# Kernel optimization log

Hardware: AMD Instinct MI355X
Metric: run time of the kernel (lower is better)

## Reference

```python
import jax, jax.numpy as jnp
import numpy as np

D_MODEL = 512
N_HEADS = 8
D_HEAD = D_MODEL // N_HEADS
B, S = 4, 2048
NEG_INF = -1e9


def rel_shift(x):
    # x: [B,H,Q,K] -> Transformer-XL relative shift
    b, h, q, k = x.shape
    x = jnp.pad(x, ((0, 0), (0, 0), (0, 0), (1, 0)))  # [B,H,Q,K+1]
    x = x.reshape(b, h, k + 1, q)[:, :, 1:, :]          # drop first row
    return x.reshape(b, h, q, k)


def setup_inputs() -> dict:
    key = jax.random.key(0)
    ks = jax.random.split(key, 9)
    sc = 1.0 / np.sqrt(D_MODEL)
    return {
        "x": jax.random.normal(ks[0], (B, S, D_MODEL), jnp.float32),
        "pos_emb": jax.random.normal(ks[1], (S, D_MODEL), jnp.float32),
        "Wq": jax.random.normal(ks[2], (D_MODEL, D_MODEL), jnp.float32) * sc,
        "Wk": jax.random.normal(ks[3], (D_MODEL, D_MODEL), jnp.float32) * sc,
        "Wv": jax.random.normal(ks[4], (D_MODEL, D_MODEL), jnp.float32) * sc,
        "Wr": jax.random.normal(ks[5], (D_MODEL, D_MODEL), jnp.float32) * sc,
        "Wo": jax.random.normal(ks[6], (D_MODEL, D_MODEL), jnp.float32) * sc,
        "u_bias": jax.random.normal(ks[7], (N_HEADS, D_HEAD), jnp.float32) * 0.02,
        "v_bias": jax.random.normal(ks[8], (N_HEADS, D_HEAD), jnp.float32) * 0.02,
    }


def reference(x, pos_emb, Wq, Wk, Wv, Wr, Wo, u_bias, v_bias):
    b, s, _ = x.shape
    # projections -> [B,S,H,Dh]; relative pos -> [S,H,Dh]
    q = (x @ Wq).reshape(b, s, N_HEADS, D_HEAD)
    k = (x @ Wk).reshape(b, s, N_HEADS, D_HEAD)
    v = (x @ Wv).reshape(b, s, N_HEADS, D_HEAD)
    r = (pos_emb @ Wr).reshape(s, N_HEADS, D_HEAD)

    # content term (AC) and position term (BD, with rel shift)
    ac = jnp.einsum("bihd,bjhd->bhij", q + u_bias, k)
    bd = rel_shift(jnp.einsum("bihd,jhd->bhij", q + v_bias, r))

    scores = (ac + bd) / np.sqrt(D_HEAD)
    causal = jnp.tril(jnp.ones((s, s), bool))
    scores = jnp.where(causal, scores, NEG_INF)
    attn = jax.nn.softmax(scores, axis=-1)  # [B,H,S,S]

    out = jnp.einsum("bhij,bjhd->bihd", attn, v).reshape(b, s, D_MODEL)
    return out @ Wo
```

## Files before the change

kernel.cpp:

```cpp
#include <hip/hip_runtime.h>
#include <math.h>

#define SS 2048
#define BB 4
#define NHD 8
#define BH (BB * NHD)

typedef float f32x4 __attribute__((ext_vector_type(4)));
typedef __bf16 bf16x8 __attribute__((ext_vector_type(8)));

__device__ __forceinline__ short f2bf(float x) {
  unsigned u = __float_as_uint(x);
  unsigned r = (u + 0x7fffu + ((u >> 16) & 1u)) >> 16;
  return (short)r;
}

__device__ __forceinline__ void gld16(const void* g, void* l) {
  __builtin_amdgcn_global_load_lds(
      (const __attribute__((address_space(1))) unsigned int*)g,
      (__attribute__((address_space(3))) unsigned int*)l, 16, 0, 0);
}

__global__ void cast_bf16(const float* __restrict__ in, short* __restrict__ out) {
  int i = blockIdx.x * blockDim.x + threadIdx.x;
  float4 v = ((const float4*)in)[i];
  ((short4*)out)[i] = make_short4(f2bf(v.x), f2bf(v.y), f2bf(v.z), f2bf(v.w));
}

__global__ __launch_bounds__(256) void castT_w(
    const float* __restrict__ W0, const float* __restrict__ W1,
    const float* __restrict__ W2, const float* __restrict__ W3,
    const float* __restrict__ W4, short* __restrict__ T0, short* __restrict__ T1,
    short* __restrict__ T2, short* __restrict__ T3, short* __restrict__ T4) {
  __shared__ float t[64][65];
  const float* W;
  short* T;
  switch (blockIdx.z) {
    case 0: W = W0; T = T0; break;
    case 1: W = W1; T = T1; break;
    case 2: W = W2; T = T2; break;
    case 3: W = W3; T = T3; break;
    default: W = W4; T = T4; break;
  }
  const int k0 = blockIdx.x * 64, n0 = blockIdx.y * 64;
  const int tid = threadIdx.x;
#pragma unroll
  for (int rep = 0; rep < 4; rep++) {
    int idx = rep * 256 + tid;
    int r = idx >> 4, c4 = (idx & 15) << 2;
    float4 v = *(const float4*)&W[(size_t)(k0 + r) * 512 + n0 + c4];
    t[r][c4] = v.x; t[r][c4 + 1] = v.y; t[r][c4 + 2] = v.z; t[r][c4 + 3] = v.w;
  }
  __syncthreads();
#pragma unroll
  for (int rep = 0; rep < 4; rep++) {
    int idx = rep * 256 + tid;
    int n = idx >> 4, k4 = (idx & 15) << 2;
    short4 s = make_short4(f2bf(t[k4][n]), f2bf(t[k4 + 1][n]),
                           f2bf(t[k4 + 2][n]), f2bf(t[k4 + 3][n]));
    *(short4*)&T[(size_t)(n0 + n) * 512 + k0 + k4] = s;
  }
}

__global__ __launch_bounds__(256) void conv_vt(const short* __restrict__ Vh,
                                               short* __restrict__ Vt) {
  __shared__ short t[64][72];
  const int s0 = blockIdx.x * 64, bh = blockIdx.y, tid = threadIdx.x;
#pragma unroll
  for (int rep = 0; rep < 4; rep++) {
    int idx = rep * 256 + tid;
    int r = idx >> 4, c4 = (idx & 15) << 2;
    *(short4*)&t[r][c4] = *(const short4*)&Vh[((size_t)bh * SS + s0 + r) * 64 + c4];
  }
  __syncthreads();
#pragma unroll
  for (int rep = 0; rep < 4; rep++) {
    int idx = rep * 256 + tid;
    int d = idx >> 4, s4 = (idx & 15) << 2;
    short4 o = make_short4(t[s4][d], t[s4 + 1][d], t[s4 + 2][d], t[s4 + 3][d]);
    *(short4*)&Vt[((size_t)bh * 64 + d) * SS + s0 + s4] = o;
  }
}

template <int EPI>
__global__ __launch_bounds__(512) void mfma_gemm(
    const short* __restrict__ A, const short* __restrict__ Bt, int M,
    short* __restrict__ o0, short* __restrict__ o1,
    const float* __restrict__ bias0, const float* __restrict__ bias1,
    float* __restrict__ of) {
  __shared__ short lds[2][2][128 * 64];
  const int m0 = blockIdx.x * 128;
  const int n0 = blockIdx.y * 128;
  const int tid = threadIdx.x;
  const int lane = tid & 63;
  const int w = tid >> 6;
  const int wr = w >> 2, wc = w & 3;
  const int g = lane >> 4, li = lane & 15;

  f32x4 acc[4][2] = {};

  auto stage = [&](int buf, int k0) {
#pragma unroll
    for (int i = 0; i < 2; i++) {
      int p = (i * 512 + tid) * 16;
      int q = p ^ ((p >> 3) & 0x70);
      int row = q >> 7, col = (q & 127) >> 1;
      gld16(A + (size_t)(m0 + row) * 512 + k0 + col, (char*)&lds[buf][0][0] + p);
      gld16(Bt + (size_t)(n0 + row) * 512 + k0 + col, (char*)&lds[buf][1][0] + p);
    }
  };

  stage(0, 0);
  __syncthreads();
  int buf = 0;
  for (int t = 0; t < 8; t++) {
    if (t < 7) stage(buf ^ 1, (t + 1) * 64);
    const char* As = (const char*)&lds[buf][0][0];
    const char* Bs = (const char*)&lds[buf][1][0];
    bf16x8 af[4][2], bfr[2][2];
#pragma unroll
    for (int ks = 0; ks < 2; ks++) {
      const int cb = g * 16 + ks * 64;
#pragma unroll
      for (int mi = 0; mi < 4; mi++) {
        int row = wr * 64 + mi * 16 + li;
        af[mi][ks] = *(const bf16x8*)(As + row * 128 + (cb ^ ((row & 7) << 4)));
      }
#pragma unroll
      for (int ni = 0; ni < 2; ni++) {
        int row = wc * 32 + ni * 16 + li;
        bfr[ni][ks] = *(const bf16x8*)(Bs + row * 128 + (cb ^ ((row & 7) << 4)));
      }
    }
#pragma unroll
    for (int ks = 0; ks < 2; ks++)
#pragma unroll
      for (int mi = 0; mi < 4; mi++)
#pragma unroll
        for (int ni = 0; ni < 2; ni++)
          acc[mi][ni] = __builtin_amdgcn_mfma_f32_16x16x32_bf16(
              af[mi][ks], bfr[ni][ks], acc[mi][ni], 0, 0, 0);
    __syncthreads();
    buf ^= 1;
  }

#pragma unroll
  for (int mi = 0; mi < 4; mi++) {
#pragma unroll
    for (int ni = 0; ni < 2; ni++) {
      const int n_g = n0 + wc * 32 + ni * 16 + li;
      const int m_b = m0 + wr * 64 + mi * 16 + g * 4;
      if (EPI == 0) {
#pragma unroll
        for (int r = 0; r < 4; r++)
          of[(size_t)(m_b + r) * 512 + n_g] = acc[mi][ni][r];
      } else if (EPI == 1) {
        const float b0 = bias0[n_g], b1 = bias1[n_g];
        const int h = n_g >> 6, d = n_g & 63;
#pragma unroll
        for (int r = 0; r < 4; r++) {
          int m_g = m_b + r;
          size_t ad = ((size_t)((m_g >> 11) * NHD + h) * SS + (m_g & 2047)) * 64 + d;
          o0[ad] = f2bf(acc[mi][ni][r] + b0);
          o1[ad] = f2bf(acc[mi][ni][r] + b1);
        }
      } else {
        const int h = n_g >> 6, d = n_g & 63;
#pragma unroll
        for (int r = 0; r < 4; r++) {
          int m_g = m_b + r;
          size_t ad = ((size_t)((m_g >> 11) * NHD + h) * SS + (m_g & 2047)) * 64 + d;
          o0[ad] = f2bf(acc[mi][ni][r]);
        }
      }
    }
  }
}

__global__ __launch_bounds__(512, 4) void flash_mfma_kernel(
    const short* __restrict__ Qu_, const short* __restrict__ Qv_,
    const short* __restrict__ Kb_, const short* __restrict__ Vt_,
    const short* __restrict__ Rb_, short* __restrict__ AOb) {
  __shared__ __align__(16) float QRl[8][80 * 18];
  __shared__ __align__(16) short Pl[8][16 * 72];

  const int bx = blockIdx.x;
  const int bh = blockIdx.y;
  const int h = bh & 7;
  const int tid = threadIdx.x;
  const int w = tid >> 6;
  const int wq = w & 3;
  const int qi = (w < 4) ? (31 - bx) : bx;
  const int i0 = qi * 64;
  const int lane = tid & 63;
  const int q = lane & 15;
  const int g = lane >> 4;
  const int dsl = g * 8;

  float* qrw = QRl[w];
  short* pw = Pl[w];

  const size_t qoff = ((size_t)bh * SS + (i0 + wq * 16 + q)) * 64;
  bf16x8 quF[2], qvF[2];
  quF[0] = *(const bf16x8*)(Qu_ + qoff + dsl);
  quF[1] = *(const bf16x8*)(Qu_ + qoff + dsl + 32);
  qvF[0] = *(const bf16x8*)(Qv_ + qoff + dsl);
  qvF[1] = *(const bf16x8*)(Qv_ + qoff + dsl + 32);

  const int i_my = i0 + wq * 16 + q;

  float m = -1e30f, l = 0.f;
  f32x4 o[4] = {};

  for (int j0 = 0; j0 <= i0; j0 += 64) {
    bf16x8 vf[4][2];
    const size_t vtb = ((size_t)bh * 64) * SS + j0;
#pragma unroll
    for (int ds = 0; ds < 4; ds++)
#pragma unroll
      for (int c = 0; c < 2; c++)
        vf[ds][c] = *(const bf16x8*)(Vt_ + vtb + (size_t)(ds * 16 + q) * SS + dsl + 32 * c);

    f32x4 accS[4] = {};
    f32x4 accR[5] = {};
    const size_t kbase = ((size_t)bh * SS + j0) * 64;
    const int rb0 = SS - 16 + j0 - i0 - 16 * wq;
    const size_t rbase = (size_t)h * SS * 64;
#pragma unroll
    for (int c = 0; c < 2; c++) {
      const int dof = dsl + 32 * c;
#pragma unroll
      for (int ks = 0; ks < 4; ks++) {
        bf16x8 kf = *(const bf16x8*)(Kb_ + kbase + (size_t)(ks * 16 + q) * 64 + dof);
        accS[ks] = __builtin_amdgcn_mfma_f32_16x16x32_bf16(kf, quF[c], accS[ks], 0, 0, 0);
      }
#pragma unroll
      for (int st = 0; st < 5; st++) {
        int rrow = rb0 + st * 16 + q;
        rrow = rrow < SS ? rrow : SS - 1;
        bf16x8 rf = *(const bf16x8*)(Rb_ + rbase + (size_t)rrow * 64 + dof);
        accR[st] = __builtin_amdgcn_mfma_f32_16x16x32_bf16(rf, qvF[c], accR[st], 0, 0, 0);
      }
    }

#pragma unroll
    for (int st = 0; st < 5; st++)
#pragma unroll
      for (int r = 0; r < 4; r++)
        qrw[(st * 16 + g * 4 + r) * 18 + q] = accR[st][r];

    float sreg[4][4];
#pragma unroll
    for (int ks = 0; ks < 4; ks++)
#pragma unroll
      for (int r = 0; r < 4; r++) {
        int krow = ks * 16 + g * 4 + r;
        float qr = qrw[(krow + 15 - q) * 18 + q];
        float sc = (accS[ks][r] + qr) * 0.125f;
        sreg[ks][r] = (j0 + krow <= i_my) ? sc : -1e30f;
      }

    float bmax = sreg[0][0];
#pragma unroll
    for (int ks = 0; ks < 4; ks++)
#pragma unroll
      for (int r = 0; r < 4; r++) bmax = fmaxf(bmax, sreg[ks][r]);
    bmax = fmaxf(bmax, __shfl_xor(bmax, 16, 64));
    bmax = fmaxf(bmax, __shfl_xor(bmax, 32, 64));
    float mnew = fmaxf(m, bmax);
    float scale = __expf(m - mnew);
    float psum = 0.f;
    short4 pk[4];
#pragma unroll
    for (int ks = 0; ks < 4; ks++) {
      float p0 = __expf(sreg[ks][0] - mnew);
      float p1 = __expf(sreg[ks][1] - mnew);
      float p2 = __expf(sreg[ks][2] - mnew);
      float p3 = __expf(sreg[ks][3] - mnew);
      psum += (p0 + p1) + (p2 + p3);
      pk[ks] = make_short4(f2bf(p0), f2bf(p1), f2bf(p2), f2bf(p3));
    }
    psum += __shfl_xor(psum, 16, 64);
    psum += __shfl_xor(psum, 32, 64);
    l = l * scale + psum;
    m = mnew;

#pragma unroll
    for (int ks = 0; ks < 4; ks++)
      *(short4*)(pw + q * 72 + ks * 16 + g * 4) = pk[ks];

#pragma unroll
    for (int r = 0; r < 4; r++) {
      float sc_r = __shfl(scale, g * 4 + r, 64);
      o[0][r] *= sc_r; o[1][r] *= sc_r; o[2][r] *= sc_r; o[3][r] *= sc_r;
    }

    bf16x8 pf[2];
    pf[0] = *(const bf16x8*)(pw + q * 72 + dsl);
    pf[1] = *(const bf16x8*)(pw + q * 72 + dsl + 32);
#pragma unroll
    for (int ds = 0; ds < 4; ds++)
#pragma unroll
      for (int c = 0; c < 2; c++)
        o[ds] = __builtin_amdgcn_mfma_f32_16x16x32_bf16(pf[c], vf[ds][c], o[ds], 0, 0, 0);
  }

  const int b = bh >> 3;
  float linv = 1.f / l;
#pragma unroll
  for (int r = 0; r < 4; r++) {
    float li2 = __shfl(linv, g * 4 + r, 64);
    int irow = i0 + wq * 16 + g * 4 + r;
    short* op = AOb + ((size_t)(b * SS + irow)) * 512 + h * 64 + q;
#pragma unroll
    for (int ds = 0; ds < 4; ds++) op[ds * 16] = f2bf(o[ds][r] * li2);
  }
}

extern "C" void kernel_launch(void* const* d_in, const int* in_sizes, int n_in,
                              void* d_out, int out_size, void* d_ws,
                              size_t ws_size, hipStream_t stream) {
  const float* x   = (const float*)d_in[0];
  const float* pos = (const float*)d_in[1];
  const float* Wq  = (const float*)d_in[2];
  const float* Wk  = (const float*)d_in[3];
  const float* Wv  = (const float*)d_in[4];
  const float* Wr  = (const float*)d_in[5];
  const float* Wo  = (const float*)d_in[6];
  const float* ub  = (const float*)d_in[7];
  const float* vb  = (const float*)d_in[8];
  float* out = (float*)d_out;

  const size_t BS = (size_t)BB * SS;
  const size_t NX = BS * 512;
  const size_t NR = (size_t)SS * 512;
  const size_t NW = 512 * 512;

  short* xb  = (short*)d_ws;
  short* pb  = xb + NX;
  short* WtQ = pb + NR;
  short* WtK = WtQ + NW;
  short* WtV = WtK + NW;
  short* WtR = WtV + NW;
  short* WtO = WtR + NW;
  short* Qu  = WtO + NW;
  short* Qv  = Qu + NX;
  short* Kb  = Qv + NX;
  short* Vh  = Kb + NX;
  short* Vt  = Vh + NX;
  short* Rb  = Vt + NX;
  short* AOb = Rb + NR;

  cast_bf16<<<dim3(NX / 1024), 256, 0, stream>>>(x, xb);
  cast_bf16<<<dim3(NR / 1024), 256, 0, stream>>>(pos, pb);
  castT_w<<<dim3(8, 8, 5), 256, 0, stream>>>(Wq, Wk, Wv, Wr, Wo,
                                             WtQ, WtK, WtV, WtR, WtO);

  mfma_gemm<1><<<dim3(64, 4), 512, 0, stream>>>(xb, WtQ, 8192, Qu, Qv, ub, vb, nullptr);
  mfma_gemm<2><<<dim3(64, 4), 512, 0, stream>>>(xb, WtK, 8192, Kb, nullptr, nullptr, nullptr, nullptr);
  mfma_gemm<2><<<dim3(64, 4), 512, 0, stream>>>(xb, WtV, 8192, Vh, nullptr, nullptr, nullptr, nullptr);
  mfma_gemm<2><<<dim3(16, 4), 512, 0, stream>>>(pb, WtR, 2048, Rb, nullptr, nullptr, nullptr, nullptr);
  conv_vt<<<dim3(SS / 64, BH), 256, 0, stream>>>(Vh, Vt);

  flash_mfma_kernel<<<dim3(16, BH), 512, 0, stream>>>(Qu, Qv, Kb, Vt, Rb, AOb);

  mfma_gemm<0><<<dim3(64, 4), 512, 0, stream>>>(AOb, WtO, 8192, nullptr, nullptr, nullptr, nullptr, out);
}
```

Before: 336.6 us.

## Merge projection launches, pack QR tile to bf16, use exp2 softmax and setprio

Merges the two cast kernels into one launch and the Q/K/V projection GEMMs into a single grid with a z dimension, cutting launch count and tail effects. In the flash kernel, the per-wave relative-position scratch is stored as packed bf16 pairs instead of fp32, which shrinks LDS use, and launch bounds rise to allow more waves per CU. Softmax switches to exp2 with log2e folded into the scale, the max and sum reductions become tree-shaped, and MFMA sections are wrapped in s_setprio. Rounding the position term to bf16 adds some precision loss.

```diff
diff --git a/kernel.cpp b/kernel.cpp
--- a/kernel.cpp
+++ b/kernel.cpp
@@ -21,10 +21,20 @@
       (__attribute__((address_space(3))) unsigned int*)l, 16, 0, 0);
 }
 
-__global__ void cast_bf16(const float* __restrict__ in, short* __restrict__ out) {
+__global__ void cast_all(const float* __restrict__ x, const float* __restrict__ pos,
+                         short* __restrict__ xb, short* __restrict__ pb, int nx4) {
   int i = blockIdx.x * blockDim.x + threadIdx.x;
-  float4 v = ((const float4*)in)[i];
-  ((short4*)out)[i] = make_short4(f2bf(v.x), f2bf(v.y), f2bf(v.z), f2bf(v.w));
+  const float4* src;
+  short4* dst;
+  if (i < nx4) {
+    src = (const float4*)x + i;
+    dst = (short4*)xb + i;
+  } else {
+    src = (const float4*)pos + (i - nx4);
+    dst = (short4*)pb + (i - nx4);
+  }
+  float4 v = *src;
+  *dst = make_short4(f2bf(v.x), f2bf(v.y), f2bf(v.z), f2bf(v.w));
 }
 
 __global__ __launch_bounds__(256) void castT_w(
@@ -82,31 +92,26 @@
   }
 }
 
-template <int EPI>
-__global__ __launch_bounds__(512) void mfma_gemm(
-    const short* __restrict__ A, const short* __restrict__ Bt, int M,
-    short* __restrict__ o0, short* __restrict__ o1,
-    const float* __restrict__ bias0, const float* __restrict__ bias1,
-    float* __restrict__ of) {
-  __shared__ short lds[2][2][128 * 64];
-  const int m0 = blockIdx.x * 128;
-  const int n0 = blockIdx.y * 128;
+__device__ __forceinline__ void gemm_core(const short* __restrict__ A,
+                                          const short* __restrict__ Bt,
+                                          short* lds, int m0, int n0,
+                                          f32x4 (&acc)[4][2]) {
   const int tid = threadIdx.x;
   const int lane = tid & 63;
   const int w = tid >> 6;
   const int wr = w >> 2, wc = w & 3;
   const int g = lane >> 4, li = lane & 15;
 
-  f32x4 acc[4][2] = {};
-
   auto stage = [&](int buf, int k0) {
 #pragma unroll
     for (int i = 0; i < 2; i++) {
       int p = (i * 512 + tid) * 16;
-      int q = p ^ ((p >> 3) & 0x70);
-      int row = q >> 7, col = (q & 127) >> 1;
-      gld16(A + (size_t)(m0 + row) * 512 + k0 + col, (char*)&lds[buf][0][0] + p);
-      gld16(Bt + (size_t)(n0 + row) * 512 + k0 + col, (char*)&lds[buf][1][0] + p);
+      int qq = p ^ ((p >> 3) & 0x70);
+      int row = qq >> 7, col = (qq & 127) >> 1;
+      gld16(A + (size_t)(m0 + row) * 512 + k0 + col,
+            (char*)(lds + (size_t)buf * 2 * 8192) + p);
+      gld16(Bt + (size_t)(n0 + row) * 512 + k0 + col,
+            (char*)(lds + ((size_t)buf * 2 + 1) * 8192) + p);
     }
   };
 
@@ -115,8 +120,8 @@
   int buf = 0;
   for (int t = 0; t < 8; t++) {
     if (t < 7) stage(buf ^ 1, (t + 1) * 64);
-    const char* As = (const char*)&lds[buf][0][0];
-    const char* Bs = (const char*)&lds[buf][1][0];
+    const char* As = (const char*)(lds + (size_t)buf * 2 * 8192);
+    const char* Bs = (const char*)(lds + ((size_t)buf * 2 + 1) * 8192);
     bf16x8 af[4][2], bfr[2][2];
 #pragma unroll
     for (int ks = 0; ks < 2; ks++) {
@@ -143,9 +148,70 @@
     __syncthreads();
     buf ^= 1;
   }
-
-#pragma unroll
-  for (int mi = 0; mi < 4; mi++) {
+}
+
+__global__ __launch_bounds__(512) void proj_gemm(
+    const short* __restrict__ A, const short* __restrict__ WtQ,
+    const short* __restrict__ WtK, const short* __restrict__ WtV,
+    short* __restrict__ Qu, short* __restrict__ Qv, short* __restrict__ Kb,
+    short* __restrict__ Vh, const float* __restrict__ ub,
+    const float* __restrict__ vb) {
+  __shared__ short lds[2][2][128 * 64];
+  const int z = blockIdx.z;
+  const short* Bt = (z == 0) ? WtQ : (z == 1) ? WtK : WtV;
+  const int m0 = blockIdx.x * 128, n0 = blockIdx.y * 128;
+  f32x4 acc[4][2] = {};
+  gemm_core(A, Bt, &lds[0][0][0], m0, n0, acc);
+
+  const int tid = threadIdx.x;
+  const int lane = tid & 63;
+  const int w = tid >> 6;
+  const int wr = w >> 2, wc = w & 3;
+  const int g = lane >> 4, li = lane & 15;
+#pragma unroll
+  for (int mi = 0; mi < 4; mi++)
+#pragma unroll
+    for (int ni = 0; ni < 2; ni++) {
+      const int n_g = n0 + wc * 32 + ni * 16 + li;
+      const int m_b = m0 + wr * 64 + mi * 16 + g * 4;
+      const int h = n_g >> 6, d = n_g & 63;
+      if (z == 0) {
+        const float b0 = ub[n_g], b1 = vb[n_g];
+#pragma unroll
+        for (int r = 0; r < 4; r++) {
+          int m_g = m_b + r;
+          size_t ad = ((size_t)((m_g >> 11) * NHD + h) * SS + (m_g & 2047)) * 64 + d;
+          Qu[ad] = f2bf(acc[mi][ni][r] + b0);
+          Qv[ad] = f2bf(acc[mi][ni][r] + b1);
+        }
+      } else {
+        short* o = (z == 1) ? Kb : Vh;
+#pragma unroll
+        for (int r = 0; r < 4; r++) {
+          int m_g = m_b + r;
+          size_t ad = ((size_t)((m_g >> 11) * NHD + h) * SS + (m_g & 2047)) * 64 + d;
+          o[ad] = f2bf(acc[mi][ni][r]);
+        }
+      }
+    }
+}
+
+template <int EPI>
+__global__ __launch_bounds__(512) void mfma_gemm(
+    const short* __restrict__ A, const short* __restrict__ Bt,
+    short* __restrict__ o0, float* __restrict__ of) {
+  __shared__ short lds[2][2][128 * 64];
+  const int m0 = blockIdx.x * 128, n0 = blockIdx.y * 128;
+  f32x4 acc[4][2] = {};
+  gemm_core(A, Bt, &lds[0][0][0], m0, n0, acc);
+
+  const int tid = threadIdx.x;
+  const int lane = tid & 63;
+  const int w = tid >> 6;
+  const int wr = w >> 2, wc = w & 3;
+  const int g = lane >> 4, li = lane & 15;
+#pragma unroll
+  for (int mi = 0; mi < 4; mi++)
 #pragma unroll
     for (int ni = 0; ni < 2; ni++) {
       const int n_g = n0 + wc * 32 + ni * 16 + li;
@@ -154,16 +220,6 @@
 #pragma unroll
         for (int r = 0; r < 4; r++)
           of[(size_t)(m_b + r) * 512 + n_g] = acc[mi][ni][r];
-      } else if (EPI == 1) {
-        const float b0 = bias0[n_g], b1 = bias1[n_g];
-        const int h = n_g >> 6, d = n_g & 63;
-#pragma unroll
-        for (int r = 0; r < 4; r++) {
-          int m_g = m_b + r;
-          size_t ad = ((size_t)((m_g >> 11) * NHD + h) * SS + (m_g & 2047)) * 64 + d;
-          o0[ad] = f2bf(acc[mi][ni][r] + b0);
-          o1[ad] = f2bf(acc[mi][ni][r] + b1);
-        }
       } else {
         const int h = n_g >> 6, d = n_g & 63;
 #pragma unroll
@@ -174,14 +230,15 @@
         }
       }
     }
-  }
-}
-
-__global__ __launch_bounds__(512, 4) void flash_mfma_kernel(
+}
+
+#define SC2 0.18033688f
+
+__global__ __launch_bounds__(512, 6) void flash_mfma_kernel(
     const short* __restrict__ Qu_, const short* __restrict__ Qv_,
     const short* __restrict__ Kb_, const short* __restrict__ Vt_,
     const short* __restrict__ Rb_, short* __restrict__ AOb) {
-  __shared__ __align__(16) float QRl[8][80 * 18];
+  __shared__ __align__(16) unsigned QRl2[8][40 * 25];
   __shared__ __align__(16) short Pl[8][16 * 72];
 
   const int bx = blockIdx.x;
@@ -197,7 +254,7 @@
   const int g = lane >> 4;
   const int dsl = g * 8;
 
-  float* qrw = QRl[w];
+  unsigned* qrw = QRl2[w];
   short* pw = Pl[w];
 
   const size_t qoff = ((size_t)bh * SS + (i0 + wq * 16 + q)) * 64;
@@ -226,6 +283,7 @@
     const size_t kbase = ((size_t)bh * SS + j0) * 64;
     const int rb0 = SS - 16 + j0 - i0 - 16 * wq;
     const size_t rbase = (size_t)h * SS * 64;
+    __builtin_amdgcn_s_setprio(1);
 #pragma unroll
     for (int c = 0; c < 2; c++) {
       const int dof = dsl + 32 * c;
@@ -242,12 +300,18 @@
         accR[st] = __builtin_amdgcn_mfma_f32_16x16x32_bf16(rf, qvF[c], accR[st], 0, 0, 0);
       }
     }
-
-#pragma unroll
-    for (int st = 0; st < 5; st++)
-#pragma unroll
-      for (int r = 0; r < 4; r++)
-        qrw[(st * 16 + g * 4 + r) * 18 + q] = accR[st][r];
+    __builtin_amdgcn_s_setprio(0);
+
+#pragma unroll
+    for (int st = 0; st < 5; st++) {
+      unsigned w01 = (unsigned)(unsigned short)f2bf(accR[st][0]) |
+                     ((unsigned)(unsigned short)f2bf(accR[st][1]) << 16);
+      unsigned w23 = (unsigned)(unsigned short)f2bf(accR[st][2]) |
+                     ((unsigned)(unsigned short)f2bf(accR[st][3]) << 16);
+      int row = st * 8 + g * 2;
+      qrw[row * 25 + q] = w01;
+      qrw[(row + 1) * 25 + q] = w23;
+    }
 
     float sreg[4][4];
 #pragma unroll
@@ -255,31 +319,35 @@
 #pragma unroll
       for (int r = 0; r < 4; r++) {
         int krow = ks * 16 + g * 4 + r;
-        float qr = qrw[(krow + 15 - q) * 18 + q];
-        float sc = (accS[ks][r] + qr) * 0.125f;
+        int t = krow + 15 - q;
+        unsigned wv = qrw[(t >> 1) * 25 + q];
+        unsigned bits = (t & 1) ? (wv & 0xffff0000u) : (wv << 16);
+        float qr = __uint_as_float(bits);
+        float sc = (accS[ks][r] + qr) * SC2;
         sreg[ks][r] = (j0 + krow <= i_my) ? sc : -1e30f;
       }
 
-    float bmax = sreg[0][0];
-#pragma unroll
-    for (int ks = 0; ks < 4; ks++)
-#pragma unroll
-      for (int r = 0; r < 4; r++) bmax = fmaxf(bmax, sreg[ks][r]);
+    float b0 = fmaxf(fmaxf(sreg[0][0], sreg[0][1]), fmaxf(sreg[0][2], sreg[0][3]));
+    float b1 = fmaxf(fmaxf(sreg[1][0], sreg[1][1]), fmaxf(sreg[1][2], sreg[1][3]));
+    float b2 = fmaxf(fmaxf(sreg[2][0], sreg[2][1]), fmaxf(sreg[2][2], sreg[2][3]));
+    float b3 = fmaxf(fmaxf(sreg[3][0], sreg[3][1]), fmaxf(sreg[3][2], sreg[3][3]));
+    float bmax = fmaxf(fmaxf(b0, b1), fmaxf(b2, b3));
     bmax = fmaxf(bmax, __shfl_xor(bmax, 16, 64));
     bmax = fmaxf(bmax, __shfl_xor(bmax, 32, 64));
     float mnew = fmaxf(m, bmax);
-    float scale = __expf(m - mnew);
-    float psum = 0.f;
+    float scale = __builtin_amdgcn_exp2f(m - mnew);
+    float ps[4];
     short4 pk[4];
 #pragma unroll
     for (int ks = 0; ks < 4; ks++) {
-      float p0 = __expf(sreg[ks][0] - mnew);
-      float p1 = __expf(sreg[ks][1] - mnew);
-      float p2 = __expf(sreg[ks][2] - mnew);
-      float p3 = __expf(sreg[ks][3] - mnew);
-      psum += (p0 + p1) + (p2 + p3);
+      float p0 = __builtin_amdgcn_exp2f(sreg[ks][0] - mnew);
+      float p1 = __builtin_amdgcn_exp2f(sreg[ks][1] - mnew);
+      float p2 = __builtin_amdgcn_exp2f(sreg[ks][2] - mnew);
+      float p3 = __builtin_amdgcn_exp2f(sreg[ks][3] - mnew);
+      ps[ks] = (p0 + p1) + (p2 + p3);
       pk[ks] = make_short4(f2bf(p0), f2bf(p1), f2bf(p2), f2bf(p3));
     }
+    float psum = (ps[0] + ps[1]) + (ps[2] + ps[3]);
     psum += __shfl_xor(psum, 16, 64);
     psum += __shfl_xor(psum, 32, 64);
     l = l * scale + psum;
@@ -298,11 +366,13 @@
     bf16x8 pf[2];
     pf[0] = *(const bf16x8*)(pw + q * 72 + dsl);
     pf[1] = *(const bf16x8*)(pw + q * 72 + dsl + 32);
+    __builtin_amdgcn_s_setprio(1);
 #pragma unroll
     for (int ds = 0; ds < 4; ds++)
 #pragma unroll
       for (int c = 0; c < 2; c++)
         o[ds] = __builtin_amdgcn_mfma_f32_16x16x32_bf16(pf[c], vf[ds][c], o[ds], 0, 0, 0);
+    __builtin_amdgcn_s_setprio(0);
   }
 
   const int b = bh >> 3;
@@ -351,18 +421,16 @@
   short* Rb  = Vt + NX;
   short* AOb = Rb + NR;
 
-  cast_bf16<<<dim3(NX / 1024), 256, 0, stream>>>(x, xb);
-  cast_bf16<<<dim3(NR / 1024), 256, 0, stream>>>(pos, pb);
+  cast_all<<<dim3((NX + NR) / 4 / 256), 256, 0, stream>>>(x, pos, xb, pb, (int)(NX / 4));
   castT_w<<<dim3(8, 8, 5), 256, 0, stream>>>(Wq, Wk, Wv, Wr, Wo,
                                              WtQ, WtK, WtV, WtR, WtO);
 
-  mfma_gemm<1><<<dim3(64, 4), 512, 0, stream>>>(xb, WtQ, 8192, Qu, Qv, ub, vb, nullptr);
-  mfma_gemm<2><<<dim3(64, 4), 512, 0, stream>>>(xb, WtK, 8192, Kb, nullptr, nullptr, nullptr, nullptr);
-  mfma_gemm<2><<<dim3(64, 4), 512, 0, stream>>>(xb, WtV, 8192, Vh, nullptr, nullptr, nullptr, nullptr);
-  mfma_gemm<2><<<dim3(16, 4), 512, 0, stream>>>(pb, WtR, 2048, Rb, nullptr, nullptr, nullptr, nullptr);
+  proj_gemm<<<dim3(64, 4, 3), 512, 0, stream>>>(xb, WtQ, WtK, WtV,
+                                                Qu, Qv, Kb, Vh, ub, vb);
+  mfma_gemm<2><<<dim3(16, 4), 512, 0, stream>>>(pb, WtR, Rb, nullptr);
   conv_vt<<<dim3(SS / 64, BH), 256, 0, stream>>>(Vh, Vt);
 
   flash_mfma_kernel<<<dim3(16, BH), 512, 0, stream>>>(Qu, Qv, Kb, Vt, Rb, AOb);
 
-  mfma_gemm<0><<<dim3(64, 4), 512, 0, stream>>>(AOb, WtO, 8192, nullptr, nullptr, nullptr, nullptr, out);
-}
+  mfma_gemm<0><<<dim3(64, 4), 512, 0, stream>>>(AOb, WtO, nullptr, out);
+}
```

New measurement: 666.8 us. 98.1% more time.
